# Performance work log

Measured on AMD Instinct MI355X. Metric: run time of the kernel, lower is better.

Reference implementation:

```python
import jax, jax.numpy as jnp
import numpy as np

A = 0.7071067811865476  # sqrt(2)/2
B_ = 1.0 - A
KH = KW = 3
K2 = 9
STRIDE = 1
PAD = 1
DIL = 1


def setup_inputs() -> dict:
    key = jax.random.key(0)
    k1, k2, k3, k4 = jax.random.split(key, 4)
    Bn, Cin, H, W = 4, 256, 64, 64
    Cout = 256
    x = jax.random.normal(k1, (Bn, Cin, H, W), dtype=jnp.float32)
    offset = jax.random.normal(k2, (Bn, 2 * K2, H, W), dtype=jnp.float32)
    mask = jax.random.uniform(k3, (Bn, K2, H, W), dtype=jnp.float32)
    stdv = 1.0 / np.sqrt(Cin * KH * KW)
    weight = jax.random.uniform(k4, (Cout, Cin, KH, KW), dtype=jnp.float32,
                                minval=-stdv, maxval=stdv)
    bias = jnp.zeros((Cout,), dtype=jnp.float32)
    return {"input": x, "offset": offset, "mask": mask, "weight": weight, "bias": bias}


def _weight_circle(weight):
    # Blend 3x3 corner taps along the diagonal "circle", as in DCNv2_Circle.forward.
    O, C = weight.shape[0], weight.shape[1]
    w = weight.reshape(O, C, K2)
    w0 = A * (A * w[:, :, 0] + B_ * w[:, :, 1]) + B_ * (A * w[:, :, 3] + B_ * w[:, :, 4])
    w2 = A * (B_ * w[:, :, 1] + A * w[:, :, 2]) + B_ * (B_ * w[:, :, 4] + A * w[:, :, 5])
    w6 = B_ * (A * w[:, :, 3] + B_ * w[:, :, 4]) + A * (A * w[:, :, 6] + B_ * w[:, :, 7])
    w8 = B_ * (B_ * w[:, :, 4] + A * w[:, :, 5]) + A * (B_ * w[:, :, 7] + A * w[:, :, 8])
    return jnp.stack([w0, w[:, :, 1], w2, w[:, :, 3], w[:, :, 4],
                      w[:, :, 5], w6, w[:, :, 7], w8], axis=-1)  # [O, C, 9]


def _dcn_v2(x, offset, mask, w_flat, bias):
    Bn, C, H, W = x.shape
    Ho = (H + 2 * PAD - DIL * (KH - 1) - 1) // STRIDE + 1
    Wo = (W + 2 * PAD - DIL * (KW - 1) - 1) // STRIDE + 1
    # Base sampling grid per kernel tap k: [K2, Ho, Wo]
    ki, kj = jnp.meshgrid(jnp.arange(KH), jnp.arange(KW), indexing="ij")
    ki = ki.reshape(K2).astype(jnp.float32)
    kj = kj.reshape(K2).astype(jnp.float32)
    oy = (jnp.arange(Ho, dtype=jnp.float32) * STRIDE - PAD)
    ox = (jnp.arange(Wo, dtype=jnp.float32) * STRIDE - PAD)
    base_y = oy[None, :, None] + DIL * ki[:, None, None]  # [K2, Ho, 1]
    base_x = ox[None, None, :] + DIL * kj[:, None, None]  # [K2, 1, Wo]
    # Offsets: channel 2k is dy, 2k+1 is dx (DCNv2 layout).
    off = offset.reshape(Bn, K2, 2, Ho, Wo)
    y = base_y[None] + off[:, :, 0]  # [B, K2, Ho, Wo]
    x_ = base_x[None] + off[:, :, 1]
    y0 = jnp.floor(y)
    x0 = jnp.floor(x_)
    ly = y - y0
    lx = x_ - x0
    y0i = y0.astype(jnp.int32)
    x0i = x0.astype(jnp.int32)
    flat = x.reshape(Bn, C, H * W)

    def gather(yi, xi):
        valid = (yi >= 0) & (yi < H) & (xi >= 0) & (xi < W)
        idx = jnp.clip(yi, 0, H - 1) * W + jnp.clip(xi, 0, W - 1)  # [B,K2,Ho,Wo]
        v = jax.vmap(lambda f, i: f[:, i.reshape(-1)])(flat, idx)  # [B,C,K2*Ho*Wo]
        v = v.reshape(Bn, C, K2, Ho, Wo)
        return v * valid[:, None].astype(v.dtype)

    hy = 1.0 - ly
    hx = 1.0 - lx
    # corner weights broadcast over channel dim
    sampled = (gather(y0i, x0i) * (hy * hx)[:, None]
               + gather(y0i, x0i + 1) * (hy * lx)[:, None]
               + gather(y0i + 1, x0i) * (ly * hx)[:, None]
               + gather(y0i + 1, x0i + 1) * (ly * lx)[:, None])  # [B,C,K2,Ho,Wo]
    sampled = sampled * mask[:, None]  # modulation
    out = jnp.einsum("bckhw,ock->bohw", sampled, w_flat)
    return out + bias[None, :, None, None]


def reference(input, offset, mask, weight, bias):
    w_flat = _weight_circle(weight)
    return _dcn_v2(input, offset, mask, w_flat, bias)
```

## Files before the change

### kernel.cpp

```cpp
#include <hip/hip_runtime.h>

typedef __bf16 bf16x8 __attribute__((ext_vector_type(8)));
typedef float f32x4 __attribute__((ext_vector_type(4)));

#define HH 64
#define WW 64
#define CIN 256
#define COUT 256
#define HW 4096
#define BSTRIDE 296
#define NROWS 12
#define XROW 65

__global__ __launch_bounds__(256) void prep_weights(const float* __restrict__ weight,
                                                    __bf16* __restrict__ wp) {
    const int idx = blockIdx.x * 256 + threadIdx.x;
    const int o   = idx >> 5;
    const int g8  = idx & 31;
    const int cg  = g8 >> 2, q = g8 & 3;
    const int c0  = cg * 32 + q * 8;
    const int tm  = o >> 4, rr = o & 15;
    const int lane = rr | (q << 4);
    const float Af = 0.70710678118654752f;
    const float Bf = 1.0f - Af;
    float r[9][8];
    #pragma unroll
    for (int j = 0; j < 8; ++j) {
        const float* w = weight + ((size_t)o * 256 + c0 + j) * 9;
        float t0=w[0],t1=w[1],t2=w[2],t3=w[3],t4=w[4],t5=w[5],t6=w[6],t7=w[7],t8=w[8];
        r[0][j] = Af*(Af*t0+Bf*t1) + Bf*(Af*t3+Bf*t4);
        r[1][j] = t1; r[3][j] = t3; r[4][j] = t4; r[5][j] = t5; r[7][j] = t7;
        r[2][j] = Af*(Bf*t1+Af*t2) + Bf*(Bf*t4+Af*t5);
        r[6][j] = Bf*(Af*t3+Bf*t4) + Af*(Af*t6+Bf*t7);
        r[8][j] = Bf*(Bf*t4+Af*t5) + Af*(Bf*t7+Af*t8);
    }
    #pragma unroll
    for (int tap = 0; tap < 9; ++tap) {
        int ksg = cg * 9 + tap;
        bf16x8 v;
        #pragma unroll
        for (int j = 0; j < 8; ++j) v[j] = (__bf16)r[tap][j];
        *(bf16x8*)&wp[(size_t)(((ksg * 16 + tm) << 6) | lane) << 3] = v;
    }
}

__global__ __launch_bounds__(512, 2) void dcn_main(
        const float* __restrict__ x, const float* __restrict__ off,
        const float* __restrict__ msk, const __bf16* __restrict__ wp,
        const float* __restrict__ bias, float* __restrict__ out) {
    __shared__ __bf16 Bs[64 * BSTRIDE];
    __shared__ __bf16 Xs[2 * NROWS * XROW * 8];

    const int tid  = threadIdx.x;
    const int wv   = tid >> 6;
    const int lane = tid & 63;
    const int q    = lane >> 4, rr = lane & 15;
    const int px   = tid & 63;
    const int c0   = wv;

    const int bid = blockIdx.x;
    const int xcd = bid & 7;
    const int r_  = bid >> 3;
    const int b   = xcd >> 1;
    const int h   = ((xcd & 1) << 5) | r_;

    const int rowbase = min(max(h - 5, 0), HH - NROWS);
    const float* xb = x + (size_t)b * CIN * HW;

    float W00[3], W01[3], W10[3], W11[3];
    int AY0[3], AY1[3], DXO[3], COLB[3], GP[3];
    #pragma unroll
    for (int k = 0; k < 3; ++k) {
        int c = c0 + k * 8;
        if (c < 18) {
            int sg = c / 9, tap = c % 9;
            int ki = tap / 3, kj = tap - 3 * ki;
            const float* offp = off + (size_t)b * 18 * HW + h * 64 + px;
            float dy = offp[(2 * tap) * HW];
            float dx = offp[(2 * tap + 1) * HW];
            float mv = msk[(size_t)b * 9 * HW + (size_t)tap * HW + h * 64 + px];
            float py  = (float)(h - 1 + ki) + dy;
            float pxf = (float)(px - 1 + kj) + dx;
            float y0f = floorf(py), x0f = floorf(pxf);
            float ly = py - y0f, lx = pxf - x0f;
            float hy = 1.0f - ly, hx = 1.0f - lx;
            int y0 = (int)y0f, x0 = (int)x0f;
            int y1 = y0 + 1, x1 = x0 + 1;
            bool vy0 = (y0 >= 0) && (y0 < HH), vy1 = (y1 >= 0) && (y1 < HH);
            bool vx0 = (x0 >= 0) && (x0 < WW), vx1 = (x1 >= 0) && (x1 < WW);
            int cy0 = min(max(y0, 0), HH - 1), cy1 = min(max(y1, 0), HH - 1);
            int cx0 = min(max(x0, 0), WW - 1), cx1 = min(max(x1, 0), WW - 1);
            W00[k] = (vy0 && vx0) ? hy * hx * mv : 0.0f;
            W01[k] = (vy0 && vx1) ? hy * lx * mv : 0.0f;
            W10[k] = (vy1 && vx0) ? ly * hx * mv : 0.0f;
            W11[k] = (vy1 && vx1) ? ly * lx * mv : 0.0f;
            int ry0 = min(max(cy0 - rowbase, 0), NROWS - 1);
            int ry1 = min(max(cy1 - rowbase, 0), NROWS - 1);
            bool useG = (vy0 && (cy0 < rowbase || cy0 > rowbase + NROWS - 1))
                     || (vy1 && (cy1 < rowbase || cy1 > rowbase + NROWS - 1));
            AY0[k]  = ((sg * NROWS + ry0) * XROW + cx0) * 16;
            AY1[k]  = ((sg * NROWS + ry1) * XROW + cx0) * 16;
            DXO[k]  = (cx1 - cx0) * 16;
            COLB[k] = (tap * 32 + sg * 8) * 2;
            GP[k]   = cy0 | (cy1 << 6) | (cx0 << 12) | (cx1 << 18) | (sg << 24)
                    | (useG ? (1u << 31) : 0);
        }
    }

    f32x4 acc[2][4];
    #pragma unroll
    for (int i = 0; i < 2; ++i)
        #pragma unroll
        for (int jj = 0; jj < 4; ++jj)
            acc[i][jj] = (f32x4)0.0f;

    const char* XsB = (const char*)Xs;
    char* BsB = (char*)Bs;

    for (int cg = 0; cg < 8; ++cg) {
        #pragma unroll
        for (int half = 0; half < 2; ++half) {
            __syncthreads();
            {
                const int ch = tid >> 5;
                const int p5 = tid & 31;
                const int sg = ch >> 3, c8 = ch & 7;
                const float* xc = xb + (size_t)(cg * 32 + half * 16 + ch) * HW
                                + rowbase * 64;
                #pragma unroll
                for (int k = 0; k < 24; ++k) {
                    int linear = k * 32 + p5;
                    float f = xc[linear];
                    int row = linear >> 6, ppx = linear & 63;
                    Xs[(((sg * NROWS + row) * XROW + ppx) << 3) + c8] = (__bf16)f;
                }
            }
            __syncthreads();
            #pragma unroll
            for (int k = 0; k < 3; ++k) {
                int c = c0 + k * 8;
                if (c < 18) {
                    bf16x8 c00 = *(const bf16x8*)(XsB + AY0[k]);
                    bf16x8 c01 = *(const bf16x8*)(XsB + AY0[k] + DXO[k]);
                    bf16x8 c10 = *(const bf16x8*)(XsB + AY1[k]);
                    bf16x8 c11 = *(const bf16x8*)(XsB + AY1[k] + DXO[k]);
                    float w0 = W00[k], w1 = W01[k], w2 = W10[k], w3 = W11[k];
                    bf16x8 res;
                    #pragma unroll
                    for (int j = 0; j < 8; ++j) {
                        float v = w0 * (float)c00[j] + w1 * (float)c01[j]
                                + w2 * (float)c10[j] + w3 * (float)c11[j];
                        res[j] = (__bf16)v;
                    }
                    int gp = GP[k];
                    if (gp < 0) {
                        int cy0 = gp & 63, cy1 = (gp >> 6) & 63;
                        int cx0 = (gp >> 12) & 63, cx1 = (gp >> 18) & 63;
                        int sg = (gp >> 24) & 3;
                        const float* xc = xb + (size_t)(cg * 32 + half * 16 + sg * 8) * HW;
                        int i00 = cy0 * 64 + cx0, i01 = cy0 * 64 + cx1;
                        int i10 = cy1 * 64 + cx0, i11 = cy1 * 64 + cx1;
                        #pragma unroll
                        for (int j = 0; j < 8; ++j) {
                            float v = w0 * xc[i00] + w1 * xc[i01]
                                    + w2 * xc[i10] + w3 * xc[i11];
                            res[j] = (__bf16)v;
                            xc += HW;
                        }
                    }
                    *(bf16x8*)(BsB + px * 592 + COLB[k] + half * 32) = res;
                }
            }
        }
        __syncthreads();
        const __bf16* ap = wp + (((size_t)(cg * 9) * 16 + wv * 2) * 64 + lane) * 8;
        bf16x8 a0 = *(const bf16x8*)ap;
        bf16x8 a1 = *(const bf16x8*)(ap + 512);
        #pragma unroll 1
        for (int kl = 0; kl < 9; ++kl) {
            bf16x8 na0 = a0, na1 = a1;
            if (kl < 8) {
                const __bf16* np = ap + 8192;
                na0 = *(const bf16x8*)np;
                na1 = *(const bf16x8*)(np + 512);
            }
            const int kcol = kl * 32 + q * 8;
            bf16x8 bb0 = *(const bf16x8*)&Bs[(0  + rr) * BSTRIDE + kcol];
            bf16x8 bb1 = *(const bf16x8*)&Bs[(16 + rr) * BSTRIDE + kcol];
            bf16x8 bb2 = *(const bf16x8*)&Bs[(32 + rr) * BSTRIDE + kcol];
            bf16x8 bb3 = *(const bf16x8*)&Bs[(48 + rr) * BSTRIDE + kcol];
            acc[0][0] = __builtin_amdgcn_mfma_f32_16x16x32_bf16(a0, bb0, acc[0][0], 0, 0, 0);
            acc[1][0] = __builtin_amdgcn_mfma_f32_16x16x32_bf16(a1, bb0, acc[1][0], 0, 0, 0);
            acc[0][1] = __builtin_amdgcn_mfma_f32_16x16x32_bf16(a0, bb1, acc[0][1], 0, 0, 0);
            acc[1][1] = __builtin_amdgcn_mfma_f32_16x16x32_bf16(a1, bb1, acc[1][1], 0, 0, 0);
            acc[0][2] = __builtin_amdgcn_mfma_f32_16x16x32_bf16(a0, bb2, acc[0][2], 0, 0, 0);
            acc[1][2] = __builtin_amdgcn_mfma_f32_16x16x32_bf16(a1, bb2, acc[1][2], 0, 0, 0);
            acc[0][3] = __builtin_amdgcn_mfma_f32_16x16x32_bf16(a0, bb3, acc[0][3], 0, 0, 0);
            acc[1][3] = __builtin_amdgcn_mfma_f32_16x16x32_bf16(a1, bb3, acc[1][3], 0, 0, 0);
            ap += 8192;
            a0 = na0;
            a1 = na1;
        }
    }

    const int mbase = wv * 32;
    #pragma unroll
    for (int tm = 0; tm < 2; ++tm) {
        #pragma unroll
        for (int i = 0; i < 4; ++i) {
            const int m = mbase + tm * 16 + q * 4 + i;
            const float bv = bias[m];
            float* op = out + ((size_t)b * COUT + m) * HW + h * 64;
            #pragma unroll
            for (int tn = 0; tn < 4; ++tn) {
                op[tn * 16 + rr] = acc[tm][tn][i] + bv;
            }
        }
    }
}

extern "C" void kernel_launch(void* const* d_in, const int* in_sizes, int n_in,
                              void* d_out, int out_size, void* d_ws, size_t ws_size,
                              hipStream_t stream) {
    const float* x      = (const float*)d_in[0];
    const float* off    = (const float*)d_in[1];
    const float* msk    = (const float*)d_in[2];
    const float* weight = (const float*)d_in[3];
    const float* bias   = (const float*)d_in[4];
    float* out = (float*)d_out;

    __bf16* wp = (__bf16*)d_ws;

    prep_weights<<<32, 256, 0, stream>>>(weight, wp);
    dcn_main<<<256, 512, 0, stream>>>(x, off, msk, wp, bias, out);
}
```

Baseline: 136.1 us.

## Prefetch input slices into registers, split MFMA K across waves, parallelize weight prep

The main kernel now loads the next 16-channel input slice into registers while the current slice is written to shared memory and sampled, so global-load latency overlaps the bilinear gather. The GEMM is repartitioned: each wave computes a 64x64 output tile over half of the nine taps, and partial sums are reduced through shared memory in the epilogue. The sampling work is rebalanced so tap columns spread more evenly across waves. The weight-prep kernel runs one thread per output vector with 288 blocks instead of 32. This costs more registers (24 prefetch floats, 64 accumulator floats) under launch_bounds(512,2), plus an extra shared-memory reduction and a barrier.

```diff
diff --git a/kernel.cpp b/kernel.cpp
--- a/kernel.cpp
+++ b/kernel.cpp
@@ -11,52 +11,67 @@
 #define BSTRIDE 296
 #define NROWS 12
 #define XROW 65
+#define XS_OFF 37888
+
+__device__ __forceinline__ void bar_sync() {
+    asm volatile("s_waitcnt lgkmcnt(0)" ::: "memory");
+    __builtin_amdgcn_s_barrier();
+    asm volatile("" ::: "memory");
+}
 
 __global__ __launch_bounds__(256) void prep_weights(const float* __restrict__ weight,
                                                     __bf16* __restrict__ wp) {
-    const int idx = blockIdx.x * 256 + threadIdx.x;
-    const int o   = idx >> 5;
-    const int g8  = idx & 31;
-    const int cg  = g8 >> 2, q = g8 & 3;
-    const int c0  = cg * 32 + q * 8;
-    const int tm  = o >> 4, rr = o & 15;
-    const int lane = rr | (q << 4);
+    const int t = blockIdx.x * 256 + threadIdx.x;
+    const int lane = t & 63;
+    const int tm   = (t >> 6) & 15;
+    const int cg   = (t >> 10) & 7;
+    const int tap  = t >> 13;
+    const int rr = lane & 15, q = lane >> 4;
+    const int o  = tm * 16 + rr;
+    const int c0 = cg * 32 + q * 8;
+    const float* wb = weight + ((size_t)o * 256 + c0) * 9;
     const float Af = 0.70710678118654752f;
     const float Bf = 1.0f - Af;
-    float r[9][8];
+    bf16x8 v;
     #pragma unroll
     for (int j = 0; j < 8; ++j) {
-        const float* w = weight + ((size_t)o * 256 + c0 + j) * 9;
-        float t0=w[0],t1=w[1],t2=w[2],t3=w[3],t4=w[4],t5=w[5],t6=w[6],t7=w[7],t8=w[8];
-        r[0][j] = Af*(Af*t0+Bf*t1) + Bf*(Af*t3+Bf*t4);
-        r[1][j] = t1; r[3][j] = t3; r[4][j] = t4; r[5][j] = t5; r[7][j] = t7;
-        r[2][j] = Af*(Bf*t1+Af*t2) + Bf*(Bf*t4+Af*t5);
-        r[6][j] = Bf*(Af*t3+Bf*t4) + Af*(Af*t6+Bf*t7);
-        r[8][j] = Bf*(Bf*t4+Af*t5) + Af*(Bf*t7+Af*t8);
-    }
-    #pragma unroll
-    for (int tap = 0; tap < 9; ++tap) {
-        int ksg = cg * 9 + tap;
-        bf16x8 v;
-        #pragma unroll
-        for (int j = 0; j < 8; ++j) v[j] = (__bf16)r[tap][j];
-        *(bf16x8*)&wp[(size_t)(((ksg * 16 + tm) << 6) | lane) << 3] = v;
-    }
+        const float* w = wb + j * 9;
+        float r;
+        switch (tap) {
+            case 0:  r = Af*(Af*w[0]+Bf*w[1]) + Bf*(Af*w[3]+Bf*w[4]); break;
+            case 1:  r = w[1]; break;
+            case 2:  r = Af*(Bf*w[1]+Af*w[2]) + Bf*(Bf*w[4]+Af*w[5]); break;
+            case 3:  r = w[3]; break;
+            case 4:  r = w[4]; break;
+            case 5:  r = w[5]; break;
+            case 6:  r = Bf*(Af*w[3]+Bf*w[4]) + Af*(Af*w[6]+Bf*w[7]); break;
+            case 7:  r = w[7]; break;
+            default: r = Bf*(Bf*w[4]+Af*w[5]) + Af*(Bf*w[7]+Af*w[8]); break;
+        }
+        v[j] = (__bf16)r;
+    }
+    const int ksg = cg * 9 + tap;
+    *(bf16x8*)&wp[(size_t)(((ksg * 16 + tm) << 6) | lane) << 3] = v;
 }
 
 __global__ __launch_bounds__(512, 2) void dcn_main(
         const float* __restrict__ x, const float* __restrict__ off,
         const float* __restrict__ msk, const __bf16* __restrict__ wp,
         const float* __restrict__ bias, float* __restrict__ out) {
-    __shared__ __bf16 Bs[64 * BSTRIDE];
-    __shared__ __bf16 Xs[2 * NROWS * XROW * 8];
+    __shared__ char smem[65536];
+    __bf16* Bs = (__bf16*)smem;
+    __bf16* Xs = (__bf16*)(smem + XS_OFF);
+    char* BsB  = smem;
+    const char* XsB = (const char*)(smem + XS_OFF);
 
     const int tid  = threadIdx.x;
     const int wv   = tid >> 6;
     const int lane = tid & 63;
     const int q    = lane >> 4, rr = lane & 15;
-    const int px   = tid & 63;
-    const int c0   = wv;
+    const int px   = lane;
+    const int ch   = tid >> 5;
+    const int p5   = tid & 31;
+    const int sgch = ch >> 3, c8 = ch & 7;
 
     const int bid = blockIdx.x;
     const int xcd = bid & 7;
@@ -69,10 +84,12 @@
 
     float W00[3], W01[3], W10[3], W11[3];
     int AY0[3], AY1[3], DXO[3], COLB[3], GP[3];
+    bool UV[3];
     #pragma unroll
     for (int k = 0; k < 3; ++k) {
-        int c = c0 + k * 8;
-        if (c < 18) {
+        int c = (k < 2) ? (wv + 8 * k) : ((wv >= 6) ? wv + 10 : -1);
+        UV[k] = (c >= 0);
+        if (UV[k]) {
             int sg = c / 9, tap = c % 9;
             int ki = tap / 3, kj = tap - 3 * ki;
             const float* offp = off + (size_t)b * 18 * HW + h * 64 + px;
@@ -107,113 +124,146 @@
         }
     }
 
-    f32x4 acc[2][4];
+    f32x4 acc[4][4];
     #pragma unroll
-    for (int i = 0; i < 2; ++i)
-        #pragma unroll
-        for (int jj = 0; jj < 4; ++jj)
-            acc[i][jj] = (f32x4)0.0f;
-
-    const char* XsB = (const char*)Xs;
-    char* BsB = (char*)Bs;
-
-    for (int cg = 0; cg < 8; ++cg) {
-        #pragma unroll
-        for (int half = 0; half < 2; ++half) {
-            __syncthreads();
-            {
-                const int ch = tid >> 5;
-                const int p5 = tid & 31;
-                const int sg = ch >> 3, c8 = ch & 7;
-                const float* xc = xb + (size_t)(cg * 32 + half * 16 + ch) * HW
-                                + rowbase * 64;
+    for (int i = 0; i < 4; ++i)
+        #pragma unroll
+        for (int n = 0; n < 4; ++n)
+            acc[i][n] = (f32x4)0.0f;
+
+    const int tm0   = (wv & 3) * 4;
+    const int klbeg = (wv & 4) ? 5 : 0;
+    const int nkl   = (wv & 4) ? 4 : 5;
+
+    float R[24];
+    {
+        const float* xc = xb + (size_t)ch * HW + rowbase * 64 + p5;
+        #pragma unroll
+        for (int k = 0; k < 24; ++k) R[k] = xc[k * 32];
+    }
+
+    for (int s = 0; s < 16; ++s) {
+        const int cg = s >> 1, half = s & 1;
+        bar_sync();
+        #pragma unroll
+        for (int k = 0; k < 24; ++k) {
+            int linear = k * 32 + p5;
+            int row = linear >> 6, ppx = linear & 63;
+            Xs[(((sgch * NROWS + row) * XROW + ppx) << 3) + c8] = (__bf16)R[k];
+        }
+        if (s < 15) {
+            const int s1 = s + 1;
+            const float* xc = xb + (size_t)(((s1 >> 1) * 32 + (s1 & 1) * 16) + ch) * HW
+                            + rowbase * 64 + p5;
+            #pragma unroll
+            for (int k = 0; k < 24; ++k) R[k] = xc[k * 32];
+        }
+        bar_sync();
+        #pragma unroll
+        for (int k = 0; k < 3; ++k) {
+            if (UV[k]) {
+                bf16x8 c00 = *(const bf16x8*)(XsB + AY0[k]);
+                bf16x8 c01 = *(const bf16x8*)(XsB + AY0[k] + DXO[k]);
+                bf16x8 c10 = *(const bf16x8*)(XsB + AY1[k]);
+                bf16x8 c11 = *(const bf16x8*)(XsB + AY1[k] + DXO[k]);
+                float w0 = W00[k], w1 = W01[k], w2 = W10[k], w3 = W11[k];
+                bf16x8 res;
                 #pragma unroll
-                for (int k = 0; k < 24; ++k) {
-                    int linear = k * 32 + p5;
-                    float f = xc[linear];
-                    int row = linear >> 6, ppx = linear & 63;
-                    Xs[(((sg * NROWS + row) * XROW + ppx) << 3) + c8] = (__bf16)f;
-                }
-            }
-            __syncthreads();
-            #pragma unroll
-            for (int k = 0; k < 3; ++k) {
-                int c = c0 + k * 8;
-                if (c < 18) {
-                    bf16x8 c00 = *(const bf16x8*)(XsB + AY0[k]);
-                    bf16x8 c01 = *(const bf16x8*)(XsB + AY0[k] + DXO[k]);
-                    bf16x8 c10 = *(const bf16x8*)(XsB + AY1[k]);
-                    bf16x8 c11 = *(const bf16x8*)(XsB + AY1[k] + DXO[k]);
-                    float w0 = W00[k], w1 = W01[k], w2 = W10[k], w3 = W11[k];
-                    bf16x8 res;
+                for (int j = 0; j < 8; ++j) {
+                    float v = w0 * (float)c00[j] + w1 * (float)c01[j]
+                            + w2 * (float)c10[j] + w3 * (float)c11[j];
+                    res[j] = (__bf16)v;
+                }
+                int gp = GP[k];
+                if (gp < 0) {
+                    int cy0 = gp & 63, cy1 = (gp >> 6) & 63;
+                    int cx0 = (gp >> 12) & 63, cx1 = (gp >> 18) & 63;
+                    int sg = (gp >> 24) & 3;
+                    const float* xc = xb + (size_t)(cg * 32 + half * 16 + sg * 8) * HW;
+                    int i00 = cy0 * 64 + cx0, i01 = cy0 * 64 + cx1;
+                    int i10 = cy1 * 64 + cx0, i11 = cy1 * 64 + cx1;
                     #pragma unroll
                     for (int j = 0; j < 8; ++j) {
-                        float v = w0 * (float)c00[j] + w1 * (float)c01[j]
-                                + w2 * (float)c10[j] + w3 * (float)c11[j];
+                        float v = w0 * xc[i00] + w1 * xc[i01]
+                                + w2 * xc[i10] + w3 * xc[i11];
                         res[j] = (__bf16)v;
+                        xc += HW;
                     }
-                    int gp = GP[k];
-                    if (gp < 0) {
-                        int cy0 = gp & 63, cy1 = (gp >> 6) & 63;
-                        int cx0 = (gp >> 12) & 63, cx1 = (gp >> 18) & 63;
-                        int sg = (gp >> 24) & 3;
-                        const float* xc = xb + (size_t)(cg * 32 + half * 16 + sg * 8) * HW;
-                        int i00 = cy0 * 64 + cx0, i01 = cy0 * 64 + cx1;
-                        int i10 = cy1 * 64 + cx0, i11 = cy1 * 64 + cx1;
-                        #pragma unroll
-                        for (int j = 0; j < 8; ++j) {
-                            float v = w0 * xc[i00] + w1 * xc[i01]
-                                    + w2 * xc[i10] + w3 * xc[i11];
-                            res[j] = (__bf16)v;
-                            xc += HW;
-                        }
-                    }
-                    *(bf16x8*)(BsB + px * 592 + COLB[k] + half * 32) = res;
-                }
+                }
+                *(bf16x8*)(BsB + px * 592 + COLB[k] + half * 32) = res;
             }
         }
-        __syncthreads();
-        const __bf16* ap = wp + (((size_t)(cg * 9) * 16 + wv * 2) * 64 + lane) * 8;
-        bf16x8 a0 = *(const bf16x8*)ap;
-        bf16x8 a1 = *(const bf16x8*)(ap + 512);
-        #pragma unroll 1
-        for (int kl = 0; kl < 9; ++kl) {
-            bf16x8 na0 = a0, na1 = a1;
-            if (kl < 8) {
-                const __bf16* np = ap + 8192;
-                na0 = *(const bf16x8*)np;
-                na1 = *(const bf16x8*)(np + 512);
+        if (half) {
+            bar_sync();
+            const __bf16* ap = wp + ((size_t)((cg * 9 + klbeg) * 16 + tm0) * 64 + lane) * 8;
+            bf16x8 a0 = *(const bf16x8*)ap;
+            bf16x8 a1 = *(const bf16x8*)(ap + 512);
+            bf16x8 a2 = *(const bf16x8*)(ap + 1024);
+            bf16x8 a3 = *(const bf16x8*)(ap + 1536);
+            int kc = (klbeg * 32 + q * 8) * 2;
+            #pragma unroll 1
+            for (int t = 0; t < nkl; ++t) {
+                bf16x8 n0 = a0, n1 = a1, n2 = a2, n3 = a3;
+                if (t + 1 < nkl) {
+                    const __bf16* np = ap + 8192;
+                    n0 = *(const bf16x8*)np;
+                    n1 = *(const bf16x8*)(np + 512);
+                    n2 = *(const bf16x8*)(np + 1024);
+                    n3 = *(const bf16x8*)(np + 1536);
+                }
+                const char* bp = BsB + rr * 592 + kc;
+                bf16x8 bb0 = *(const bf16x8*)(bp);
+                bf16x8 bb1 = *(const bf16x8*)(bp + 16 * 592);
+                bf16x8 bb2 = *(const bf16x8*)(bp + 32 * 592);
+                bf16x8 bb3 = *(const bf16x8*)(bp + 48 * 592);
+                acc[0][0] = __builtin_amdgcn_mfma_f32_16x16x32_bf16(a0, bb0, acc[0][0], 0, 0, 0);
+                acc[1][0] = __builtin_amdgcn_mfma_f32_16x16x32_bf16(a1, bb0, acc[1][0], 0, 0, 0);
+                acc[2][0] = __builtin_amdgcn_mfma_f32_16x16x32_bf16(a2, bb0, acc[2][0], 0, 0, 0);
+                acc[3][0] = __builtin_amdgcn_mfma_f32_16x16x32_bf16(a3, bb0, acc[3][0], 0, 0, 0);
+                acc[0][1] = __builtin_amdgcn_mfma_f32_16x16x32_bf16(a0, bb1, acc[0][1], 0, 0, 0);
+                acc[1][1] = __builtin_amdgcn_mfma_f32_16x16x32_bf16(a1, bb1, acc[1][1], 0, 0, 0);
+                acc[2][1] = __builtin_amdgcn_mfma_f32_16x16x32_bf16(a2, bb1, acc[2][1], 0, 0, 0);
+                acc[3][1] = __builtin_amdgcn_mfma_f32_16x16x32_bf16(a3, bb1, acc[3][1], 0, 0, 0);
+                acc[0][2] = __builtin_amdgcn_mfma_f32_16x16x32_bf16(a0, bb2, acc[0][2], 0, 0, 0);
+                acc[1][2] = __builtin_amdgcn_mfma_f32_16x16x32_bf16(a1, bb2, acc[1][2], 0, 0, 0);
+                acc[2][2] = __builtin_amdgcn_mfma_f32_16x16x32_bf16(a2, bb2, acc[2][2], 0, 0, 0);
+                acc[3][2] = __builtin_amdgcn_mfma_f32_16x16x32_bf16(a3, bb2, acc[3][2], 0, 0, 0);
+                acc[0][3] = __builtin_amdgcn_mfma_f32_16x16x32_bf16(a0, bb3, acc[0][3], 0, 0, 0);
+                acc[1][3] = __builtin_amdgcn_mfma_f32_16x16x32_bf16(a1, bb3, acc[1][3], 0, 0, 0);
+                acc[2][3] = __builtin_amdgcn_mfma_f32_16x16x32_bf16(a2, bb3, acc[2][3], 0, 0, 0);
+                acc[3][3] = __builtin_amdgcn_mfma_f32_16x16x32_bf16(a3, bb3, acc[3][3], 0, 0, 0);
+                ap += 8192;
+                kc += 64;
+                a0 = n0; a1 = n1; a2 = n2; a3 = n3;
             }
-            const int kcol = kl * 32 + q * 8;
-            bf16x8 bb0 = *(const bf16x8*)&Bs[(0  + rr) * BSTRIDE + kcol];
-            bf16x8 bb1 = *(const bf16x8*)&Bs[(16 + rr) * BSTRIDE + kcol];
-            bf16x8 bb2 = *(const bf16x8*)&Bs[(32 + rr) * BSTRIDE + kcol];
-            bf16x8 bb3 = *(const bf16x8*)&Bs[(48 + rr) * BSTRIDE + kcol];
-            acc[0][0] = __builtin_amdgcn_mfma_f32_16x16x32_bf16(a0, bb0, acc[0][0], 0, 0, 0);
-            acc[1][0] = __builtin_amdgcn_mfma_f32_16x16x32_bf16(a1, bb0, acc[1][0], 0, 0, 0);
-            acc[0][1] = __builtin_amdgcn_mfma_f32_16x16x32_bf16(a0, bb1, acc[0][1], 0, 0, 0);
-            acc[1][1] = __builtin_amdgcn_mfma_f32_16x16x32_bf16(a1, bb1, acc[1][1], 0, 0, 0);
-            acc[0][2] = __builtin_amdgcn_mfma_f32_16x16x32_bf16(a0, bb2, acc[0][2], 0, 0, 0);
-            acc[1][2] = __builtin_amdgcn_mfma_f32_16x16x32_bf16(a1, bb2, acc[1][2], 0, 0, 0);
-            acc[0][3] = __builtin_amdgcn_mfma_f32_16x16x32_bf16(a0, bb3, acc[0][3], 0, 0, 0);
-            acc[1][3] = __builtin_amdgcn_mfma_f32_16x16x32_bf16(a1, bb3, acc[1][3], 0, 0, 0);
-            ap += 8192;
-            a0 = na0;
-            a1 = na1;
-        }
-    }
-
-    const int mbase = wv * 32;
-    #pragma unroll
-    for (int tm = 0; tm < 2; ++tm) {
+        }
+    }
+
+    float* scr = (float*)smem;
+    bar_sync();
+    if (wv >= 4) {
+        const int base = (wv - 4) * 4096 + lane * 4;
+        #pragma unroll
+        for (int i = 0; i < 4; ++i)
+            #pragma unroll
+            for (int n = 0; n < 4; ++n)
+                *(f32x4*)&scr[base + (i * 4 + n) * 256] = acc[i][n];
+    }
+    bar_sync();
+    if (wv < 4) {
+        const int mrow = wv * 64;
+        const int base = wv * 4096 + lane * 4;
         #pragma unroll
         for (int i = 0; i < 4; ++i) {
-            const int m = mbase + tm * 16 + q * 4 + i;
-            const float bv = bias[m];
-            float* op = out + ((size_t)b * COUT + m) * HW + h * 64;
             #pragma unroll
-            for (int tn = 0; tn < 4; ++tn) {
-                op[tn * 16 + rr] = acc[tm][tn][i] + bv;
+            for (int n = 0; n < 4; ++n) {
+                f32x4 p = *(const f32x4*)&scr[base + (i * 4 + n) * 256];
+                #pragma unroll
+                for (int e = 0; e < 4; ++e) {
+                    int m = mrow + i * 16 + q * 4 + e;
+                    out[((size_t)b * COUT + m) * HW + h * 64 + n * 16 + rr]
+                        = acc[i][n][e] + p[e] + bias[m];
+                }
             }
         }
     }
@@ -231,6 +281,6 @@
 
     __bf16* wp = (__bf16*)d_ws;
 
-    prep_weights<<<32, 256, 0, stream>>>(weight, wp);
+    prep_weights<<<288, 256, 0, stream>>>(weight, wp);
     dcn_main<<<256, 512, 0, stream>>>(x, off, msk, wp, bias, out);
 }
```

After: 131.6 us. -3.3%, faster.
